# Optimization experiments

Measured on AMD Instinct MI355X. Metric: run time of the kernel, lower is better.

## Reference

```python
import jax, jax.numpy as jnp
import numpy as np
from jax import lax

B, C, H, W, D = 2, 64, 32, 32, 32
N = H * W * D          # input_size = 32768
P = 64                 # proj_size
NH = 4                 # num_heads
HD = C // NH           # head dim = 16
LN_EPS = 1e-5
BN_EPS = 1e-5


def setup_inputs() -> dict:
    key = jax.random.key(0)
    ks = jax.random.split(key, 10)
    s = lambda k, shape: (jax.random.normal(k, shape, jnp.float32) * 0.02)
    return dict(
        x=jax.random.normal(ks[0], (B, C, H, W, D), jnp.float32),
        ln_w=jnp.ones((C,), jnp.float32), ln_b=jnp.zeros((C,), jnp.float32),
        gamma=1e-6 * jnp.ones((C,), jnp.float32),
        temp1=jnp.ones((NH, 1, 1), jnp.float32),
        temp2=jnp.ones((NH, 1, 1), jnp.float32),
        W_qkvv=s(ks[1], (4 * C, C)),                      # Linear(C,4C), no bias
        W_EF=s(ks[2], (P, N)), b_EF=jnp.zeros((P,), jnp.float32),  # shared E=F
        W_o1=s(ks[3], (C // 2, C)), b_o1=jnp.zeros((C // 2,), jnp.float32),
        W_o2=s(ks[4], (C // 2, C)), b_o2=jnp.zeros((C // 2,), jnp.float32),
        conv1_w=s(ks[5], (C, C, 3, 3, 3)),
        conv2_w=s(ks[6], (C, C, 3, 3, 3)),
        bn1_w=jnp.ones((C,), jnp.float32), bn1_b=jnp.zeros((C,), jnp.float32),
        bn2_w=jnp.ones((C,), jnp.float32), bn2_b=jnp.zeros((C,), jnp.float32),
        conv8_w=s(ks[7], (C, C, 1, 1, 1)), conv8_b=jnp.zeros((C,), jnp.float32),
    )


def _ln(x, w, b):
    mu = jnp.mean(x, axis=-1, keepdims=True)
    var = jnp.mean(jnp.square(x - mu), axis=-1, keepdims=True)
    return (x - mu) * lax.rsqrt(var + LN_EPS) * w + b


def _l2norm(x):  # F.normalize(dim=-1), eps=1e-12
    n = jnp.sqrt(jnp.sum(jnp.square(x), axis=-1, keepdims=True))
    return x / jnp.maximum(n, 1e-12)


def _bn_eval(x, w, b):  # BatchNorm3d in eval mode, running mean 0 / var 1
    scale = (w * lax.rsqrt(jnp.float32(1.0 + BN_EPS))).reshape(1, -1, 1, 1, 1)
    return x * scale + b.reshape(1, -1, 1, 1, 1)


def _conv3d(x, w, pad):
    return lax.conv_general_dilated(
        x, w, window_strides=(1, 1, 1), padding=[(pad, pad)] * 3,
        dimension_numbers=('NCDHW', 'OIDHW', 'NCDHW'))


def _lrelu(x):
    return jnp.where(x >= 0, x, 0.01 * x)


def _epa(xn, W_qkvv, W_EF, b_EF, temp1, temp2, W_o1, b_o1, W_o2, b_o2):
    b, n, c = xn.shape
    qkvv = (xn @ W_qkvv.T).reshape(b, n, 4, NH, HD).transpose(2, 0, 3, 1, 4)  # [4,B,h,N,d]
    q, k, v_ca, v_sa = [jnp.swapaxes(qkvv[i], -2, -1) for i in range(4)]      # [B,h,d,N]
    # shared linear projection E = F over the token axis N -> P
    k_proj = jnp.einsum('bhdn,pn->bhdp', k, W_EF) + b_EF
    v_proj = jnp.einsum('bhdn,pn->bhdp', v_sa, W_EF) + b_EF
    qn, kn = _l2norm(q), _l2norm(k)
    # channel attention: [B,h,d,d]
    attn_ca = jax.nn.softmax(jnp.einsum('bhdn,bhen->bhde', qn, kn) * temp1, axis=-1)
    x_ca = jnp.einsum('bhde,bhen->bhdn', attn_ca, v_ca)                       # [B,h,d,N]
    x_ca = x_ca.transpose(0, 3, 1, 2).reshape(b, n, c)
    # spatial attention with projected K/V: [B,h,N,P]
    attn_sa = jax.nn.softmax(jnp.einsum('bhdn,bhdp->bhnp', qn, k_proj) * temp2, axis=-1)
    x_sa = jnp.einsum('bhnp,bhdp->bhnd', attn_sa, v_proj)                     # [B,h,N,d]
    # faithful to original UNETR++ code: permute(0,3,1,2) then reshape(B,N,C)
    x_sa = x_sa.transpose(0, 3, 1, 2).reshape(b, n, c)
    x_sa = x_sa @ W_o1.T + b_o1
    x_ca = x_ca @ W_o2.T + b_o2
    return jnp.concatenate([x_sa, x_ca], axis=-1)


def reference(x, ln_w, ln_b, gamma, temp1, temp2, W_qkvv, W_EF, b_EF,
              W_o1, b_o1, W_o2, b_o2, conv1_w, conv2_w,
              bn1_w, bn1_b, bn2_w, bn2_b, conv8_w, conv8_b):
    b, c, h, w, d = x.shape
    xs = x.reshape(b, c, h * w * d).transpose(0, 2, 1)  # [B,N,C]
    attn = xs + gamma * _epa(_ln(xs, ln_w, ln_b), W_qkvv, W_EF, b_EF,
                             temp1, temp2, W_o1, b_o1, W_o2, b_o2)
    attn_skip = attn.reshape(b, h, w, d, c).transpose(0, 4, 1, 2, 3)  # [B,C,H,W,D]
    # UnetResBlock (stride 1, in==out -> identity residual), BN in eval mode
    out = _lrelu(_bn_eval(_conv3d(attn_skip, conv1_w, 1), bn1_w, bn1_b))
    out = _bn_eval(_conv3d(out, conv2_w, 1), bn2_w, bn2_b)
    out = _lrelu(out + attn_skip)
    # conv8: Dropout3d (off, eval) + 1x1x1 conv with bias
    y = _conv3d(out, conv8_w, 0) + conv8_b.reshape(1, -1, 1, 1, 1)
    return attn_skip + y
```

## Files before the change

### kernel.cpp

```cpp
#include <hip/hip_runtime.h>

#define NTOK 32768

typedef __attribute__((ext_vector_type(8))) short short8;
typedef __attribute__((ext_vector_type(4))) short short4_t;
typedef __attribute__((ext_vector_type(4))) float f32x4;

__device__ __forceinline__ short f2b(float f) {
    union { float f; unsigned u; } v; v.f = f;
    unsigned r = v.u + 0x7fffu + ((v.u >> 16) & 1u);
    return (short)(r >> 16);
}
__device__ __forceinline__ float b2f(short s) {
    union { float f; unsigned u; } v;
    v.u = ((unsigned)(unsigned short)s) << 16;
    return v.f;
}

__global__ void k_repack(const float* __restrict__ w1, const float* __restrict__ w2,
                         const float* __restrict__ w8, const float* __restrict__ wef,
                         const float* __restrict__ wq, const float* __restrict__ bEF,
                         short* __restrict__ wb1, short* __restrict__ wb2,
                         short* __restrict__ wb8, short* __restrict__ wefb,
                         short* __restrict__ wqb, float* __restrict__ kp,
                         float* __restrict__ vp, float* __restrict__ qd)
{
    int i = blockIdx.x * 256 + threadIdx.x;
    if (i >= 2349312) return;
    if (i >= 2347008) { qd[i - 2347008] = 0.f; return; }
    if (i >= 2338816) {
        int j = i - 2338816;
        float v = bEF[j & 63];
        kp[j] = v; vp[j] = v; return;
    }
    if (i >= 2322432) { int j = i - 2322432; wqb[j] = f2b(wq[j]); return; }
    if (i >= 225280)  { int j = i - 225280;  wefb[j] = f2b(wef[j]); return; }
    if (i >= 221184)  { int j = i - 221184;  wb8[j] = f2b(w8[j]); return; }
    int sel = i >= 110592;
    int j = sel ? i - 110592 : i;
    int tap = j >> 12;
    int r = j & 4095;
    int oc = r >> 6, ic = r & 63;
    const float* w = sel ? w2 : w1;
    short* o = sel ? wb2 : wb1;
    o[j] = f2b(w[(oc * 64 + ic) * 27 + tap]);
}

__global__ __launch_bounds__(256) void k_ln_qkvv(
    const float* __restrict__ x, const float* __restrict__ lnw,
    const float* __restrict__ lnb, const short* __restrict__ wqb,
    short* __restrict__ qkvvb)
{
    __shared__ __align__(16) short Wl[256 * 72];
    __shared__ __align__(16) short tr[256 * 72];
    __shared__ float red1[4][64], red2[4][64];
    __shared__ float mu_s[64], rs_s[64];
    short* al = tr;

    int bid = blockIdx.x;
    int b = bid >> 9;
    int n0 = (bid & 511) << 6;
    int tid = threadIdx.x;

    for (int i = tid; i < 2048; i += 256) {
        int out = i >> 3, q8 = (i & 7) * 8;
        *(short8*)&Wl[out * 72 + q8] = *(const short8*)&wqb[out * 64 + q8];
    }

    int t = tid & 63, cq = tid >> 6;
    float xr[16];
    float s1 = 0.f, s2 = 0.f;
    const float* xb = x + (((size_t)(b * 64 + cq * 16)) << 15) + n0 + t;
#pragma unroll
    for (int j = 0; j < 16; ++j) {
        float v = xb[(size_t)j << 15];
        xr[j] = v; s1 += v; s2 += v * v;
    }
    red1[cq][t] = s1; red2[cq][t] = s2;
    __syncthreads();
    if (tid < 64) {
        float a = red1[0][tid] + red1[1][tid] + red1[2][tid] + red1[3][tid];
        float q = red2[0][tid] + red2[1][tid] + red2[2][tid] + red2[3][tid];
        float mu = a * (1.f / 64.f);
        float var = q * (1.f / 64.f) - mu * mu;
        mu_s[tid] = mu;
        rs_s[tid] = rsqrtf(var + 1e-5f);
    }
    __syncthreads();
    {
        float mu = mu_s[t], rs = rs_s[t];
        short8 p0, p1;
#pragma unroll
        for (int j = 0; j < 8; ++j) {
            int c = cq * 16 + j;
            p0[j] = f2b((xr[j] - mu) * rs * lnw[c] + lnb[c]);
        }
#pragma unroll
        for (int j = 0; j < 8; ++j) {
            int c = cq * 16 + 8 + j;
            p1[j] = f2b((xr[8 + j] - mu) * rs * lnw[c] + lnb[c]);
        }
        *(short8*)&al[t * 72 + cq * 16] = p0;
        *(short8*)&al[t * 72 + cq * 16 + 8] = p1;
    }
    __syncthreads();

    int w = tid >> 6, lane = tid & 63, l15 = lane & 15, quad = lane >> 4;
    f32x4 acc[4][4];
#pragma unroll
    for (int mt = 0; mt < 4; ++mt)
#pragma unroll
        for (int nt = 0; nt < 4; ++nt) acc[mt][nt] = (f32x4){0.f, 0.f, 0.f, 0.f};
#pragma unroll
    for (int ks = 0; ks < 2; ++ks) {
        short8 af[4], bf[4];
#pragma unroll
        for (int mt = 0; mt < 4; ++mt)
            af[mt] = *(const short8*)&al[(mt * 16 + l15) * 72 + quad * 8 + ks * 32];
#pragma unroll
        for (int nt = 0; nt < 4; ++nt)
            bf[nt] = *(const short8*)&Wl[(w * 64 + nt * 16 + l15) * 72 + quad * 8 + ks * 32];
#pragma unroll
        for (int mt = 0; mt < 4; ++mt)
#pragma unroll
            for (int nt = 0; nt < 4; ++nt)
                acc[mt][nt] = __builtin_amdgcn_mfma_f32_16x16x32_bf16(af[mt], bf[nt], acc[mt][nt], 0, 0, 0);
    }
    __syncthreads();

#pragma unroll
    for (int mt = 0; mt < 4; ++mt)
#pragma unroll
        for (int nt = 0; nt < 4; ++nt) {
            int out = w * 64 + nt * 16 + l15;
            short4_t sv;
#pragma unroll
            for (int r = 0; r < 4; ++r) sv[r] = f2b(acc[mt][nt][r]);
            *(short4_t*)&tr[out * 72 + mt * 16 + quad * 4] = sv;
        }
    __syncthreads();
    for (int i = tid; i < 2048; i += 256) {
        int o = i >> 3, tq = (i & 7) * 8;
        short8 v = *(const short8*)&tr[o * 72 + tq];
        int isel = o >> 6, h = (o >> 4) & 3, d = o & 15;
        *(short8*)&qkvvb[((size_t)(((isel * 2 + b) * 4 + h) * 16 + d) << 15) + n0 + tq] = v;
    }
}

__global__ __launch_bounds__(256) void k_pq(
    const short* __restrict__ qkvvb, const short* __restrict__ wefb,
    float* __restrict__ kp, float* __restrict__ vp, float* __restrict__ qd,
    float* __restrict__ qn_acc, float* __restrict__ kn_acc)
{
    __shared__ float redb[3][64][38];
    int kc = blockIdx.x, bh = blockIdx.y;
    int tid = threadIdx.x;
    int w = tid >> 6, lane = tid & 63, l15 = lane & 15, quad = lane >> 4;
    size_t qrow = ((size_t)(bh * 16 + l15)) << 15;
    size_t krow = ((size_t)(128 + bh * 16 + l15)) << 15;
    size_t vrow = ((size_t)(384 + bh * 16 + l15)) << 15;
    int nbase = kc * 512 + w * 128 + quad * 8;
    f32x4 acck[4], accv[4], accqd, accqq, acckk;
#pragma unroll
    for (int nt = 0; nt < 4; ++nt) {
        acck[nt] = (f32x4){0.f, 0.f, 0.f, 0.f};
        accv[nt] = (f32x4){0.f, 0.f, 0.f, 0.f};
    }
    accqd = (f32x4){0.f, 0.f, 0.f, 0.f};
    accqq = (f32x4){0.f, 0.f, 0.f, 0.f};
    acckk = (f32x4){0.f, 0.f, 0.f, 0.f};
#pragma unroll
    for (int ks = 0; ks < 4; ++ks) {
        int n = nbase + ks * 32;
        short8 qf = *(const short8*)&qkvvb[qrow + n];
        short8 kf = *(const short8*)&qkvvb[krow + n];
        short8 vf = *(const short8*)&qkvvb[vrow + n];
        accqd = __builtin_amdgcn_mfma_f32_16x16x32_bf16(qf, kf, accqd, 0, 0, 0);
        accqq = __builtin_amdgcn_mfma_f32_16x16x32_bf16(qf, qf, accqq, 0, 0, 0);
        acckk = __builtin_amdgcn_mfma_f32_16x16x32_bf16(kf, kf, acckk, 0, 0, 0);
#pragma unroll
        for (int nt = 0; nt < 4; ++nt) {
            short8 wf = *(const short8*)&wefb[(((size_t)(nt * 16 + l15)) << 15) + n];
            acck[nt] = __builtin_amdgcn_mfma_f32_16x16x32_bf16(kf, wf, acck[nt], 0, 0, 0);
            accv[nt] = __builtin_amdgcn_mfma_f32_16x16x32_bf16(vf, wf, accv[nt], 0, 0, 0);
        }
    }
    int diag = (quad == (l15 >> 2));
    float qqv = diag ? accqq[l15 & 3] : 0.f;
    float kkv = diag ? acckk[l15 & 3] : 0.f;
    if (w > 0) {
        float* p = &redb[w - 1][lane][0];
#pragma unroll
        for (int nt = 0; nt < 4; ++nt)
#pragma unroll
            for (int r = 0; r < 4; ++r) { p[nt * 4 + r] = acck[nt][r]; p[16 + nt * 4 + r] = accv[nt][r]; }
#pragma unroll
        for (int r = 0; r < 4; ++r) p[32 + r] = accqd[r];
        p[36] = qqv; p[37] = kkv;
    }
    __syncthreads();
    if (w == 0) {
#pragma unroll
        for (int wv = 0; wv < 3; ++wv) {
            const float* p = &redb[wv][lane][0];
#pragma unroll
            for (int nt = 0; nt < 4; ++nt)
#pragma unroll
                for (int r = 0; r < 4; ++r) { acck[nt][r] += p[nt * 4 + r]; accv[nt][r] += p[16 + nt * 4 + r]; }
#pragma unroll
            for (int r = 0; r < 4; ++r) accqd[r] += p[32 + r];
            qqv += p[36]; kkv += p[37];
        }
        int d = quad * 4;
#pragma unroll
        for (int nt = 0; nt < 4; ++nt)
#pragma unroll
            for (int r = 0; r < 4; ++r) {
                int idx = (bh * 16 + d + r) * 64 + nt * 16 + l15;
                atomicAdd(&kp[idx], acck[nt][r]);
                atomicAdd(&vp[idx], accv[nt][r]);
            }
#pragma unroll
        for (int r = 0; r < 4; ++r)
            atomicAdd(&qd[bh * 256 + (d + r) * 16 + l15], accqd[r]);
        if (diag) {
            atomicAdd(&qn_acc[bh * 16 + l15], qqv);
            atomicAdd(&kn_acc[bh * 16 + l15], kkv);
        }
    }
}

__global__ __launch_bounds__(256) void k_attn(
    const short* __restrict__ qkvvb, const float* __restrict__ qd,
    const float* __restrict__ qn_acc, const float* __restrict__ kn_acc,
    const float* __restrict__ temp1, const float* __restrict__ kp,
    const float* __restrict__ vp, const float* __restrict__ temp2,
    short* __restrict__ xsab, short* __restrict__ xcab)
{
    __shared__ float kl[16][64];
    __shared__ float vl[16][64];
    __shared__ float alca[16][16];
    __shared__ float iqs[16], iks[16];
    int bh = blockIdx.y; int b = bh >> 2, h = bh & 3;
    int tid = threadIdx.x;
    for (int i = tid; i < 1024; i += 256) {
        kl[i >> 6][i & 63] = kp[bh * 1024 + i];
        vl[i >> 6][i & 63] = vp[bh * 1024 + i];
    }
    if (tid < 32) {
        int j = tid & 15;
        float v = (tid < 16) ? qn_acc[bh * 16 + j] : kn_acc[bh * 16 + j];
        float rv = 1.f / fmaxf(sqrtf(v), 1e-12f);
        if (tid < 16) iqs[j] = rv; else iks[j] = rv;
    }
    __syncthreads();
    {
        int r = tid >> 4, e = tid & 15;
        float v = qd[bh * 256 + tid] * iqs[r] * iks[e] * temp1[h];
        float mx = v;
#pragma unroll
        for (int m = 1; m < 16; m <<= 1) mx = fmaxf(mx, __shfl_xor(mx, m));
        float ex = __expf(v - mx);
        float s = ex;
#pragma unroll
        for (int m = 1; m < 16; m <<= 1) s += __shfl_xor(s, m);
        alca[r][e] = ex / s;
    }
    __syncthreads();
    int n = blockIdx.x * 256 + tid;

    {
        const short* vbase = qkvvb + (((size_t)(256 + bh * 16)) << 15) + n;
        float acc[16];
#pragma unroll
        for (int d = 0; d < 16; ++d) acc[d] = 0.f;
#pragma unroll
        for (int e = 0; e < 16; ++e) {
            float va = b2f(vbase[(size_t)e << 15]);
#pragma unroll
            for (int d = 0; d < 16; ++d) acc[d] += alca[d][e] * va;
        }
        short8 lo, hi;
#pragma unroll
        for (int j = 0; j < 8; ++j) { lo[j] = f2b(acc[j]); hi[j] = f2b(acc[j + 8]); }
        short* op = xcab + ((size_t)(b * NTOK + n)) * 64 + h * 16;
        *(short8*)&op[0] = lo;
        *(short8*)&op[8] = hi;
    }

    const short* qbase = qkvvb + (((size_t)(bh * 16)) << 15) + n;
    float qn_[16];
#pragma unroll
    for (int d = 0; d < 16; ++d) qn_[d] = b2f(qbase[(size_t)d << 15]) * iqs[d];
    float t2 = temp2[h];
    float sc[64];
#pragma unroll
    for (int p = 0; p < 64; ++p) sc[p] = 0.f;
#pragma unroll
    for (int d = 0; d < 16; ++d) {
        float qv = qn_[d];
        const float4* kr = (const float4*)&kl[d][0];
#pragma unroll
        for (int p4 = 0; p4 < 16; ++p4) {
            float4 kv = kr[p4];
            sc[p4 * 4 + 0] += qv * kv.x; sc[p4 * 4 + 1] += qv * kv.y;
            sc[p4 * 4 + 2] += qv * kv.z; sc[p4 * 4 + 3] += qv * kv.w;
        }
    }
    float mx = -1e30f;
#pragma unroll
    for (int p = 0; p < 64; ++p) { sc[p] *= t2; mx = fmaxf(mx, sc[p]); }
    float s = 0.f;
#pragma unroll
    for (int p = 0; p < 64; ++p) { sc[p] = __expf(sc[p] - mx); s += sc[p]; }
    float inv = 1.f / s;
#pragma unroll
    for (int p = 0; p < 64; ++p) sc[p] *= inv;
    short* ob = xsab + (size_t)b * 2097152 + n;
#pragma unroll
    for (int d = 0; d < 16; ++d) {
        const float4* vr = (const float4*)&vl[d][0];
        float a0 = 0, a1 = 0, a2 = 0, a3 = 0;
#pragma unroll
        for (int p4 = 0; p4 < 16; ++p4) {
            float4 vv = vr[p4];
            a0 += sc[p4 * 4] * vv.x; a1 += sc[p4 * 4 + 1] * vv.y;
            a2 += sc[p4 * 4 + 2] * vv.z; a3 += sc[p4 * 4 + 3] * vv.w;
        }
        ob[(size_t)(d * 4 + h) << 15] = f2b((a0 + a1) + (a2 + a3));
    }
}

__global__ __launch_bounds__(256) void k_epilogue(
    const float* __restrict__ x, const short* __restrict__ xsab,
    const short* __restrict__ xcab, const float* __restrict__ Wo1,
    const float* __restrict__ bo1, const float* __restrict__ Wo2,
    const float* __restrict__ bo2, const float* __restrict__ gamma,
    float* __restrict__ attn_skip, short* __restrict__ gA)
{
    __shared__ __align__(16) short Wl[64 * 72];
    __shared__ __align__(16) short trS[128 * 72];
    int tid = threadIdx.x;
    int bidx = blockIdx.x;
    int b = bidx >> 8;
    int n0 = (bidx & 255) << 7;
    for (int i = tid; i < 4096; i += 256) {
        int row = i >> 6, c = i & 63;
        float wv = (row < 32) ? Wo1[row * 64 + c] : Wo2[(row - 32) * 64 + c];
        Wl[row * 72 + c] = f2b(wv);
    }
    __syncthreads();

    int w = tid >> 6, lane = tid & 63, l15 = lane & 15, quad = lane >> 4;
    int tw = n0 + w * 32;
    const short* sa_base = xsab + (size_t)b * 2097152;
    const short* ca_base = xcab + (size_t)b * 2097152;

    f32x4 acc_sa[2][2], acc_ca[2][2];
#pragma unroll
    for (int mt = 0; mt < 2; ++mt)
#pragma unroll
        for (int nt = 0; nt < 2; ++nt) {
            acc_sa[mt][nt] = (f32x4){0.f, 0.f, 0.f, 0.f};
            acc_ca[mt][nt] = (f32x4){0.f, 0.f, 0.f, 0.f};
        }
#pragma unroll
    for (int ks = 0; ks < 2; ++ks) {
        int ko = quad * 8 + ks * 32;
        short8 b1[2], b2[2];
#pragma unroll
        for (int nt = 0; nt < 2; ++nt) {
            b1[nt] = *(const short8*)&Wl[(nt * 16 + l15) * 72 + ko];
            b2[nt] = *(const short8*)&Wl[(32 + nt * 16 + l15) * 72 + ko];
        }
#pragma unroll
        for (int mt = 0; mt < 2; ++mt) {
            int trow = tw + mt * 16 + l15;
            short8 a1 = *(const short8*)&sa_base[(size_t)trow * 64 + ko];
            short8 a2 = *(const short8*)&ca_base[(size_t)trow * 64 + ko];
#pragma unroll
            for (int nt = 0; nt < 2; ++nt) {
                acc_sa[mt][nt] = __builtin_amdgcn_mfma_f32_16x16x32_bf16(a1, b1[nt], acc_sa[mt][nt], 0, 0, 0);
                acc_ca[mt][nt] = __builtin_amdgcn_mfma_f32_16x16x32_bf16(a2, b2[nt], acc_ca[mt][nt], 0, 0, 0);
            }
        }
    }

#pragma unroll
    for (int half = 0; half < 2; ++half) {
#pragma unroll
        for (int nt = 0; nt < 2; ++nt) {
            int c = half * 32 + nt * 16 + l15;
            float g = gamma[c];
            float bias = half ? bo2[c - 32] : bo1[c];
#pragma unroll
            for (int mt = 0; mt < 2; ++mt) {
                f32x4 a = half ? acc_ca[mt][nt] : acc_sa[mt][nt];
                int tbase = tw + mt * 16 + quad * 4;
                size_t gidx = (((size_t)(b * 64 + c)) << 15) + tbase;
                f32x4 xv = *(const f32x4*)&x[gidx];
                f32x4 o;
#pragma unroll
                for (int r = 0; r < 4; ++r) {
                    float v = xv[r] + g * (a[r] + bias);
                    o[r] = v;
                    trS[(w * 32 + mt * 16 + quad * 4 + r) * 72 + c] = f2b(v);
                }
                *(f32x4*)&attn_skip[gidx] = o;
            }
        }
    }
    __syncthreads();
    for (int i = tid; i < 1024; i += 256) {
        int tok = i >> 3, cq = (i & 7) * 8;
        short8 v = *(const short8*)&trS[tok * 72 + cq];
        *(short8*)&gA[((size_t)(b * NTOK + n0 + tok)) * 64 + cq] = v;
    }
}

template <int MODE>
__global__ __launch_bounds__(256) void k_conv3m(
    const short* __restrict__ gin, const short* __restrict__ wb,
    const float* __restrict__ bnw, const float* __restrict__ bnb,
    const float* __restrict__ skip, short* __restrict__ goutS,
    const short* __restrict__ wb8, const float* __restrict__ b8,
    float* __restrict__ io)
{
    __shared__ __align__(16) short inl_s[24480];
    __shared__ __align__(16) short wl_s[15360];
    int bx = blockIdx.x;
    int bb = bx >> 8;
    int z0 = (bx >> 3) & 31;
    int y0 = (bx & 7) * 4;
    int tid = threadIdx.x;
    int lane = tid & 63, wv = tid >> 6;
    int l15 = lane & 15, quad = lane >> 4;
    int wo = tid >> 2, wq = tid & 3;

    f32x4 acc[2][4];
#pragma unroll
    for (int s = 0; s < 2; ++s)
#pragma unroll
        for (int nt = 0; nt < 4; ++nt) acc[s][nt] = (f32x4){0.f, 0.f, 0.f, 0.f};

    for (int chunk = 0; chunk < 2; ++chunk) {
        const short* wck = wb + chunk * 32 + wq * 8;
        short8 wr[3];
#pragma unroll
        for (int t = 0; t < 3; ++t)
            wr[t] = *(const short8*)&wck[(size_t)(t * 64 + wo) * 64];
        __syncthreads();
        for (int i = tid; i < 2448; i += 256) {
            int p = i >> 2, icq = i & 3;
            int xi = p % 34; int t2 = p / 34; int yi = t2 % 6; int zi = t2 / 6;
            int gz = z0 + zi - 1, gy = y0 + yi - 1, gx = xi - 1;
            short8 v = {0, 0, 0, 0, 0, 0, 0, 0};
            if ((unsigned)gz < 32u && (unsigned)gy < 32u && (unsigned)gx < 32u)
                v = *(const short8*)&gin[((size_t)(bb * NTOK + gz * 1024 + gy * 32 + gx)) * 64 + chunk * 32 + icq * 8];
            *(short8*)&inl_s[p * 40 + icq * 8] = v;
        }
#pragma unroll
        for (int t = 0; t < 3; ++t)
            *(short8*)&wl_s[(t * 64 + wo) * 40 + wq * 8] = wr[t];

#pragma unroll
        for (int kz = 0; kz < 3; ++kz)
#pragma unroll
        for (int ky = 0; ky < 3; ++ky) {
            const int sidx = kz * 3 + ky;
            __syncthreads();
            if (sidx < 8) {
#pragma unroll
                for (int t = 0; t < 3; ++t)
                    wr[t] = *(const short8*)&wck[(size_t)(((sidx + 1) * 3 + t) * 64 + wo) * 64];
            }
            const short* wcur = &wl_s[(sidx & 1) * 7680];
            int rowb = (kz * 6 + wv + ky) * 34;
#pragma unroll
            for (int kx = 0; kx < 3; ++kx) {
                short8 bf[4];
#pragma unroll
                for (int nt = 0; nt < 4; ++nt)
                    bf[nt] = *(const short8*)&wcur[(kx * 64 + nt * 16 + l15) * 40 + quad * 8];
#pragma unroll
                for (int s = 0; s < 2; ++s) {
                    short8 af = *(const short8*)&inl_s[(rowb + s * 16 + l15 + kx) * 40 + quad * 8];
#pragma unroll
                    for (int nt = 0; nt < 4; ++nt)
                        acc[s][nt] = __builtin_amdgcn_mfma_f32_16x16x32_bf16(af, bf[nt], acc[s][nt], 0, 0, 0);
                }
            }
            if (sidx < 8) {
                short* wnext = &wl_s[((sidx + 1) & 1) * 7680];
#pragma unroll
                for (int t = 0; t < 3; ++t)
                    *(short8*)&wnext[(t * 64 + wo) * 40 + wq * 8] = wr[t];
            }
        }
    }
    __syncthreads();
    float rb = rsqrtf(1.f + 1e-5f);
    if (MODE == 0) {
        short* outS = inl_s;
#pragma unroll
        for (int nt = 0; nt < 4; ++nt) {
            int oc = nt * 16 + l15;
            float sc_ = bnw[oc] * rb, sh_ = bnb[oc];
#pragma unroll
            for (int s = 0; s < 2; ++s) {
                f32x4 v = acc[s][nt];
#pragma unroll
                for (int r = 0; r < 4; ++r) {
                    int pos = wv * 32 + s * 16 + quad * 4 + r;
                    float val = v[r] * sc_ + sh_;
                    val = val >= 0.f ? val : 0.01f * val;
                    outS[pos * 72 + oc] = f2b(val);
                }
            }
        }
        __syncthreads();
        for (int i = tid; i < 1024; i += 256) {
            int p = i >> 3, cq = i & 7;
            short8 v = *(const short8*)&outS[p * 72 + cq * 8];
            int y = p >> 5, x = p & 31;
            *(short8*)&goutS[((size_t)(bb * NTOK + z0 * 1024 + (y0 + y) * 32 + x)) * 64 + cq * 8] = v;
        }
    } else {
        float* outF = (float*)inl_s;
        short* a2_s = wl_s;
        short* w8_s = wl_s + 9216;
#pragma unroll
        for (int nt = 0; nt < 4; ++nt) {
            int oc = nt * 16 + l15;
#pragma unroll
            for (int s = 0; s < 2; ++s) {
                f32x4 v = acc[s][nt];
#pragma unroll
                for (int r = 0; r < 4; ++r) {
                    int pos = wv * 32 + s * 16 + quad * 4 + r;
                    outF[oc * 132 + pos] = v[r];
                }
            }
        }
        __syncthreads();
        f32x4 skr[8];
#pragma unroll
        for (int it = 0; it < 8; ++it) {
            int i = it * 256 + tid;
            int oc = i >> 5, xq = i & 31, pos0 = xq * 4;
            f32x4 c4 = *(const f32x4*)&outF[oc * 132 + pos0];
            int y = pos0 >> 5, xx = pos0 & 31;
            size_t g = (((size_t)(bb * 64 + oc)) << 15) + ((z0 * 32 + (y0 + y)) * 32 + xx);
            f32x4 sk = *(const f32x4*)&skip[g];
            skr[it] = sk;
            float sc_ = bnw[oc] * rb, sh_ = bnb[oc];
#pragma unroll
            for (int r = 0; r < 4; ++r) {
                float val = c4[r] * sc_ + sh_ + sk[r];
                val = val >= 0.f ? val : 0.01f * val;
                a2_s[(pos0 + r) * 72 + oc] = f2b(val);
            }
        }
        for (int i = tid; i < 512; i += 256) {
            int ocw = i >> 3, cq = i & 7;
            *(short8*)&w8_s[ocw * 80 + cq * 8] = *(const short8*)&wb8[ocw * 64 + cq * 8];
        }
        __syncthreads();
        f32x4 acc2[2][4];
#pragma unroll
        for (int s = 0; s < 2; ++s)
#pragma unroll
            for (int nt = 0; nt < 4; ++nt) acc2[s][nt] = (f32x4){0.f, 0.f, 0.f, 0.f};
#pragma unroll
        for (int ks = 0; ks < 2; ++ks) {
            short8 a8[2], b8f[4];
#pragma unroll
            for (int s = 0; s < 2; ++s)
                a8[s] = *(const short8*)&a2_s[(wv * 32 + s * 16 + l15) * 72 + quad * 8 + ks * 32];
#pragma unroll
            for (int nt = 0; nt < 4; ++nt)
                b8f[nt] = *(const short8*)&w8_s[(nt * 16 + l15) * 80 + quad * 8 + ks * 32];
#pragma unroll
            for (int s = 0; s < 2; ++s)
#pragma unroll
                for (int nt = 0; nt < 4; ++nt)
                    acc2[s][nt] = __builtin_amdgcn_mfma_f32_16x16x32_bf16(a8[s], b8f[nt], acc2[s][nt], 0, 0, 0);
        }
        __syncthreads();
#pragma unroll
        for (int nt = 0; nt < 4; ++nt) {
            int oc = nt * 16 + l15;
#pragma unroll
            for (int s = 0; s < 2; ++s) {
                f32x4 v = acc2[s][nt];
#pragma unroll
                for (int r = 0; r < 4; ++r) {
                    int pos = wv * 32 + s * 16 + quad * 4 + r;
                    outF[oc * 132 + pos] = v[r];
                }
            }
        }
        __syncthreads();
#pragma unroll
        for (int it = 0; it < 8; ++it) {
            int i = it * 256 + tid;
            int oc = i >> 5, xq = i & 31, pos0 = xq * 4;
            f32x4 cv = *(const f32x4*)&outF[oc * 132 + pos0];
            int y = pos0 >> 5, xx = pos0 & 31;
            size_t g = (((size_t)(bb * 64 + oc)) << 15) + ((z0 * 32 + (y0 + y)) * 32 + xx);
            float bias8 = b8[oc];
            f32x4 o;
#pragma unroll
            for (int r = 0; r < 4; ++r) o[r] = skr[it][r] + cv[r] + bias8;
            *(f32x4*)&io[g] = o;
        }
    }
}

extern "C" void kernel_launch(void* const* d_in, const int* in_sizes, int n_in,
                              void* d_out, int out_size, void* d_ws, size_t ws_size,
                              hipStream_t stream) {
    const float* x      = (const float*)d_in[0];
    const float* ln_w   = (const float*)d_in[1];
    const float* ln_b   = (const float*)d_in[2];
    const float* gamma  = (const float*)d_in[3];
    const float* temp1  = (const float*)d_in[4];
    const float* temp2  = (const float*)d_in[5];
    const float* W_qkvv = (const float*)d_in[6];
    const float* W_EF   = (const float*)d_in[7];
    const float* b_EF   = (const float*)d_in[8];
    const float* W_o1   = (const float*)d_in[9];
    const float* b_o1   = (const float*)d_in[10];
    const float* W_o2   = (const float*)d_in[11];
    const float* b_o2   = (const float*)d_in[12];
    const float* conv1w = (const float*)d_in[13];
    const float* conv2w = (const float*)d_in[14];
    const float* bn1_w  = (const float*)d_in[15];
    const float* bn1_b  = (const float*)d_in[16];
    const float* bn2_w  = (const float*)d_in[17];
    const float* bn2_b  = (const float*)d_in[18];
    const float* conv8w = (const float*)d_in[19];
    const float* conv8b = (const float*)d_in[20];

    short* qkvvb = (short*)d_ws;
    float* kp    = (float*)(qkvvb + 16777216);
    float* vp    = kp + 8192;
    float* qd    = vp + 8192;
    float* qn_acc= qd + 2048;
    float* kn_acc= qn_acc + 128;
    float* a_ca  = kn_acc + 128;
    float* iqn   = a_ca + 2048;
    float* ikn   = iqn + 128;
    short* xcab  = (short*)(ikn + 128);
    short* xsab  = xcab + 4194304;
    short* gA    = xsab + 4194304;
    short* g1    = gA + 4194304;
    short* wb1   = g1 + 4194304;
    short* wb2   = wb1 + 110592;
    short* wb8   = wb2 + 110592;
    short* wefb  = wb8 + 4096;
    short* wqb   = wefb + 2097152;

    float* attn_skip = (float*)d_out;

    hipLaunchKernelGGL(k_repack, dim3(9177), dim3(256), 0, stream,
                       conv1w, conv2w, conv8w, W_EF, W_qkvv, b_EF,
                       wb1, wb2, wb8, wefb, wqb, kp, vp, qd);
    hipLaunchKernelGGL(k_ln_qkvv, dim3(1024), dim3(256), 0, stream,
                       x, ln_w, ln_b, wqb, qkvvb);
    hipLaunchKernelGGL(k_pq, dim3(64, 8), dim3(256), 0, stream,
                       qkvvb, wefb, kp, vp, qd, qn_acc, kn_acc);
    hipLaunchKernelGGL(k_attn, dim3(128, 8), dim3(256), 0, stream,
                       qkvvb, qd, qn_acc, kn_acc, temp1, kp, vp, temp2, xsab, xcab);
    hipLaunchKernelGGL(k_epilogue, dim3(512), dim3(256), 0, stream,
                       x, xsab, xcab, W_o1, b_o1, W_o2, b_o2, gamma, attn_skip, gA);
    hipLaunchKernelGGL((k_conv3m<0>), dim3(512), dim3(256), 0, stream,
                       gA, wb1, bn1_w, bn1_b, (const float*)nullptr, g1,
                       (const short*)nullptr, (const float*)nullptr, (float*)nullptr);
    hipLaunchKernelGGL((k_conv3m<1>), dim3(512), dim3(256), 0, stream,
                       g1, wb2, bn2_w, bn2_b, attn_skip, (short*)nullptr,
                       wb8, conv8b, attn_skip);
}
```

Measured before the change: 239.1 us.

## Rewrite k_attn spatial and channel attention with bf16 MFMA tiles

```diff
diff --git a/kernel.cpp b/kernel.cpp
--- a/kernel.cpp
+++ b/kernel.cpp
@@ -237,10 +237,12 @@
     const float* __restrict__ vp, const float* __restrict__ temp2,
     short* __restrict__ xsab, short* __restrict__ xcab)
 {
-    __shared__ float kl[16][64];
-    __shared__ float vl[16][64];
-    __shared__ float alca[16][16];
+    __shared__ float kl[16][68];
+    __shared__ float vl[16][68];
+    __shared__ float alca[16][17];
     __shared__ float iqs[16], iks[16];
+    __shared__ __align__(16) short Pl[4][64][72];
+    __shared__ short Ol[4][64][17];
     int bh = blockIdx.y; int b = bh >> 2, h = bh & 3;
     int tid = threadIdx.x;
     for (int i = tid; i < 1024; i += 256) {
@@ -267,67 +269,150 @@
         alca[r][e] = ex / s;
     }
     __syncthreads();
-    int n = blockIdx.x * 256 + tid;
-
-    {
-        const short* vbase = qkvvb + (((size_t)(256 + bh * 16)) << 15) + n;
-        float acc[16];
-#pragma unroll
-        for (int d = 0; d < 16; ++d) acc[d] = 0.f;
-#pragma unroll
-        for (int e = 0; e < 16; ++e) {
-            float va = b2f(vbase[(size_t)e << 15]);
-#pragma unroll
-            for (int d = 0; d < 16; ++d) acc[d] += alca[d][e] * va;
-        }
-        short8 lo, hi;
-#pragma unroll
-        for (int j = 0; j < 8; ++j) { lo[j] = f2b(acc[j]); hi[j] = f2b(acc[j + 8]); }
-        short* op = xcab + ((size_t)(b * NTOK + n)) * 64 + h * 16;
-        *(short8*)&op[0] = lo;
-        *(short8*)&op[8] = hi;
-    }
-
-    const short* qbase = qkvvb + (((size_t)(bh * 16)) << 15) + n;
-    float qn_[16];
-#pragma unroll
-    for (int d = 0; d < 16; ++d) qn_[d] = b2f(qbase[(size_t)d << 15]) * iqs[d];
+
+    int w = tid >> 6, lane = tid & 63, l15 = lane & 15, quad = lane >> 4;
+    int tw = (blockIdx.x << 8) + w * 64;
     float t2 = temp2[h];
-    float sc[64];
-#pragma unroll
-    for (int p = 0; p < 64; ++p) sc[p] = 0.f;
+    const short8 zero8 = {0, 0, 0, 0, 0, 0, 0, 0};
+    int xs = (l15 & 7) << 3;
+
+    short8 qb[4];
+    if (quad < 2) {
+#pragma unroll
+        for (int tnt = 0; tnt < 4; ++tnt) {
+            short8 v;
+#pragma unroll
+            for (int j = 0; j < 8; ++j) {
+                int d = quad * 8 + j;
+                short qv = qkvvb[(((size_t)(bh * 16 + d)) << 15) + tw + tnt * 16 + l15];
+                v[j] = f2b(b2f(qv) * iqs[d]);
+            }
+            qb[tnt] = v;
+        }
+    } else {
+#pragma unroll
+        for (int tnt = 0; tnt < 4; ++tnt) qb[tnt] = zero8;
+    }
+    short8 ka[4];
+    if (quad < 2) {
+#pragma unroll
+        for (int pmt = 0; pmt < 4; ++pmt) {
+            short8 v;
+#pragma unroll
+            for (int j = 0; j < 8; ++j) v[j] = f2b(kl[quad * 8 + j][pmt * 16 + l15]);
+            ka[pmt] = v;
+        }
+    } else {
+#pragma unroll
+        for (int pmt = 0; pmt < 4; ++pmt) ka[pmt] = zero8;
+    }
+
+    f32x4 st[4][4];
+#pragma unroll
+    for (int pmt = 0; pmt < 4; ++pmt)
+#pragma unroll
+        for (int tnt = 0; tnt < 4; ++tnt) st[pmt][tnt] = (f32x4){0.f, 0.f, 0.f, 0.f};
+#pragma unroll
+    for (int pmt = 0; pmt < 4; ++pmt)
+#pragma unroll
+        for (int tnt = 0; tnt < 4; ++tnt)
+            st[pmt][tnt] = __builtin_amdgcn_mfma_f32_16x16x32_bf16(ka[pmt], qb[tnt], st[pmt][tnt], 0, 0, 0);
+
+#pragma unroll
+    for (int tnt = 0; tnt < 4; ++tnt) {
+        int tok = tnt * 16 + l15;
+        float v[16];
+        float mx = -1e30f;
+#pragma unroll
+        for (int pmt = 0; pmt < 4; ++pmt)
+#pragma unroll
+            for (int r = 0; r < 4; ++r) {
+                float x = st[pmt][tnt][r] * t2;
+                v[pmt * 4 + r] = x; mx = fmaxf(mx, x);
+            }
+        mx = fmaxf(mx, __shfl_xor(mx, 16));
+        mx = fmaxf(mx, __shfl_xor(mx, 32));
+        float s = 0.f;
+#pragma unroll
+        for (int i2 = 0; i2 < 16; ++i2) { v[i2] = __expf(v[i2] - mx); s += v[i2]; }
+        s += __shfl_xor(s, 16);
+        s += __shfl_xor(s, 32);
+        float inv = 1.f / s;
+#pragma unroll
+        for (int pmt = 0; pmt < 4; ++pmt)
+#pragma unroll
+            for (int t = 0; t < 2; ++t) {
+                unsigned lo = (unsigned short)f2b(v[pmt * 4 + 2 * t] * inv);
+                unsigned hi = (unsigned short)f2b(v[pmt * 4 + 2 * t + 1] * inv);
+                int col = (pmt * 16 + quad * 4 + 2 * t) ^ xs;
+                *(unsigned*)&Pl[w][tok][col] = lo | (hi << 16);
+            }
+    }
+
+    short8 vb[2];
+#pragma unroll
+    for (int ks = 0; ks < 2; ++ks) {
+        short8 t;
+#pragma unroll
+        for (int j = 0; j < 8; ++j) t[j] = f2b(vl[l15][quad * 8 + ks * 32 + j]);
+        vb[ks] = t;
+    }
+    f32x4 vo[4];
+#pragma unroll
+    for (int mt = 0; mt < 4; ++mt) vo[mt] = (f32x4){0.f, 0.f, 0.f, 0.f};
+#pragma unroll
+    for (int mt = 0; mt < 4; ++mt) {
+        int tok = mt * 16 + l15;
+#pragma unroll
+        for (int ks = 0; ks < 2; ++ks) {
+            short8 pa = *(const short8*)&Pl[w][tok][(quad * 8 + ks * 32) ^ xs];
+            vo[mt] = __builtin_amdgcn_mfma_f32_16x16x32_bf16(pa, vb[ks], vo[mt], 0, 0, 0);
+        }
+    }
+
+    short8 ab[4], bb;
+    if (quad < 2) {
+        short8 t;
+#pragma unroll
+        for (int j = 0; j < 8; ++j) t[j] = f2b(alca[l15][quad * 8 + j]);
+        bb = t;
+#pragma unroll
+        for (int mt = 0; mt < 4; ++mt) {
+            short8 u;
+#pragma unroll
+            for (int j = 0; j < 8; ++j)
+                u[j] = qkvvb[(((size_t)(256 + bh * 16 + quad * 8 + j)) << 15) + tw + mt * 16 + l15];
+            ab[mt] = u;
+        }
+    } else {
+        bb = zero8;
+#pragma unroll
+        for (int mt = 0; mt < 4; ++mt) ab[mt] = zero8;
+    }
+    f32x4 ca[4];
+#pragma unroll
+    for (int mt = 0; mt < 4; ++mt) ca[mt] = (f32x4){0.f, 0.f, 0.f, 0.f};
+#pragma unroll
+    for (int mt = 0; mt < 4; ++mt)
+        ca[mt] = __builtin_amdgcn_mfma_f32_16x16x32_bf16(ab[mt], bb, ca[mt], 0, 0, 0);
+
+#pragma unroll
+    for (int mt = 0; mt < 4; ++mt)
+#pragma unroll
+        for (int r = 0; r < 4; ++r) {
+            int tok = tw + mt * 16 + quad * 4 + r;
+            xcab[((size_t)(b * NTOK + tok)) * 64 + h * 16 + l15] = f2b(ca[mt][r]);
+        }
+
+#pragma unroll
+    for (int mt = 0; mt < 4; ++mt)
+#pragma unroll
+        for (int r = 0; r < 4; ++r)
+            Ol[w][mt * 16 + quad * 4 + r][l15] = f2b(vo[mt][r]);
 #pragma unroll
     for (int d = 0; d < 16; ++d) {
-        float qv = qn_[d];
-        const float4* kr = (const float4*)&kl[d][0];
-#pragma unroll
-        for (int p4 = 0; p4 < 16; ++p4) {
-            float4 kv = kr[p4];
-            sc[p4 * 4 + 0] += qv * kv.x; sc[p4 * 4 + 1] += qv * kv.y;
-            sc[p4 * 4 + 2] += qv * kv.z; sc[p4 * 4 + 3] += qv * kv.w;
-        }
-    }
-    float mx = -1e30f;
-#pragma unroll
-    for (int p = 0; p < 64; ++p) { sc[p] *= t2; mx = fmaxf(mx, sc[p]); }
-    float s = 0.f;
-#pragma unroll
-    for (int p = 0; p < 64; ++p) { sc[p] = __expf(sc[p] - mx); s += sc[p]; }
-    float inv = 1.f / s;
-#pragma unroll
-    for (int p = 0; p < 64; ++p) sc[p] *= inv;
-    short* ob = xsab + (size_t)b * 2097152 + n;
-#pragma unroll
-    for (int d = 0; d < 16; ++d) {
-        const float4* vr = (const float4*)&vl[d][0];
-        float a0 = 0, a1 = 0, a2 = 0, a3 = 0;
-#pragma unroll
-        for (int p4 = 0; p4 < 16; ++p4) {
-            float4 vv = vr[p4];
-            a0 += sc[p4 * 4] * vv.x; a1 += sc[p4 * 4 + 1] * vv.y;
-            a2 += sc[p4 * 4 + 2] * vv.z; a3 += sc[p4 * 4 + 3] * vv.w;
-        }
-        ob[(size_t)(d * 4 + h) << 15] = f2b((a0 + a1) + (a2 + a3));
+        short vv = Ol[w][lane][d];
+        xsab[(size_t)b * 2097152 + (((size_t)(d * 4 + h)) << 15) + tw + lane] = vv;
     }
 }
 
```

Measured after the change: 218.0 us. 8.8% less time.
